# Kernel tuning notes

Measured on AMD Instinct MI355X. Metric: run time of the kernel, lower is better.

The kernel has to match this reference:

```python
import jax, jax.numpy as jnp
import numpy as np

B, N_IN, N_UP, SEQ, CIN, COUT = 8, 7056, 28224, 9, 64, 32
E = 3 * N_UP  # nnz of sparse upsample matrix


def setup_inputs() -> dict:
    key = jax.random.key(0)
    ks = jax.random.split(key, 7)
    x = jax.random.normal(ks[0], (B, N_IN, CIN), dtype=jnp.float32)
    val = jax.random.uniform(ks[1], (E,), dtype=jnp.float32)
    # xavier-uniform-ish init for Linear(SEQ*CIN -> COUT)
    lim = float(np.sqrt(6.0 / (SEQ * CIN + COUT)))
    W = jax.random.uniform(ks[2], (SEQ * CIN, COUT), minval=-lim, maxval=lim, dtype=jnp.float32)
    b = jnp.zeros((COUT,), dtype=jnp.float32)
    row = jax.random.randint(ks[3], (E,), 0, N_UP)
    col = jax.random.randint(ks[4], (E,), 0, N_IN)
    indices = jax.random.randint(ks[5], (N_UP, SEQ), 0, N_UP)
    return {"x": x, "val": val, "W": W, "b": b, "row": row, "col": col, "indices": indices}


def reference(x, val, W, b, row, col, indices):
    # Pool: out[b, row, :] += x[b, col, :] * val   (sparse upsample, dim_size = N_UP)
    gathered = x[:, col, :] * val[None, :, None]              # [B, E, CIN]
    pooled = jnp.zeros((x.shape[0], N_UP, x.shape[2]), dtype=x.dtype)
    pooled = pooled.at[:, row, :].add(gathered)               # [B, N_UP, CIN]
    # SpiralConv: spiral neighborhood gather then Linear + ReLU
    spiral = pooled[:, indices.reshape(-1), :]                # [B, N_UP*SEQ, CIN]
    spiral = spiral.reshape(x.shape[0], N_UP, SEQ * x.shape[2])  # [B, N_UP, SEQ*CIN]
    out = jnp.einsum('bnf,fo->bno', spiral, W) + b            # [B, N_UP, COUT]
    return jax.nn.relu(out)
```

## Files before the change

### kernel.cpp

```cpp
#include <hip/hip_runtime.h>
#include <hip/hip_bf16.h>

namespace {
constexpr int kB    = 8;
constexpr int kNIn  = 7056;
constexpr int kNUp  = 28224;
constexpr int kSeq  = 9;
constexpr int kCin  = 64;
constexpr int kCout = 32;
constexpr int kE    = 3 * kNUp;
constexpr int kMRows = kB * kNUp;
constexpr int kTilesPerB = kNUp / 16;
constexpr int kWFragN = 18 * 2 * 64 * 8;
constexpr int kCap   = 24;

constexpr size_t kOffPool   = 0;
constexpr size_t kOffWfrag  = 28901376;
constexpr size_t kOffCur    = kOffWfrag + 36864;
constexpr size_t kOffBucket = kOffCur + 112896;
}

typedef __attribute__((ext_vector_type(8))) short short8;
typedef __attribute__((ext_vector_type(4))) float f32x4;

__device__ __forceinline__ unsigned short f32_to_bf16(float f) {
    unsigned int u = __float_as_uint(f);
    u += 0x7fffu + ((u >> 16) & 1u);
    return (unsigned short)(u >> 16);
}

__global__ __launch_bounds__(256) void zero_kernel(int* __restrict__ cursor) {
    int i = blockIdx.x * 256 + threadIdx.x;
    if (i < kNUp) cursor[i] = 0;
}

__global__ __launch_bounds__(256) void prep_kernel(const float* __restrict__ W,
                                                   unsigned short* __restrict__ wfrag,
                                                   const int* __restrict__ row,
                                                   const int* __restrict__ col,
                                                   const float* __restrict__ val,
                                                   int* __restrict__ cursor,
                                                   uint2* __restrict__ bucket) {
    int bid = blockIdx.x;
    if (bid < kWFragN / 256) {
        int i  = bid * 256 + threadIdx.x;
        int j  = i & 7;
        int l  = (i >> 3) & 63;
        int ct = (i >> 9) & 1;
        int ks = i >> 10;
        int k  = ks * 32 + (l >> 4) * 8 + j;
        int o  = ct * 16 + (l & 15);
        wfrag[i] = f32_to_bf16(W[k * kCout + o]);
    } else {
        int e = (bid - kWFragN / 256) * 256 + threadIdx.x;
        if (e >= kE) return;
        int r = row[e];
        int slot = atomicAdd(&cursor[r], 1);
        if ((unsigned)slot < (unsigned)kCap)
            bucket[(size_t)r * kCap + slot] = make_uint2((unsigned)col[e], __float_as_uint(val[e]));
    }
}

__global__ __launch_bounds__(256) void pool_gather(const float* __restrict__ x,
                                                   const int* __restrict__ cursor,
                                                   const uint2* __restrict__ bucket,
                                                   unsigned short* __restrict__ poolb) {
    int t  = threadIdx.x;
    int c4 = t & 15;
    int b  = blockIdx.x & 7;
    int rb = blockIdx.x >> 3;
    int r  = rb * 16 + (t >> 4);
    int n  = min(cursor[r], kCap);
    const uint2* bk = bucket + (size_t)r * kCap;
    const float* xb = x + (size_t)b * kNIn * kCin + (size_t)c4 * 4;

    f32x4 acc = {0.f, 0.f, 0.f, 0.f};

#pragma unroll
    for (int p = 0; p < 4; ++p) {
        if (2 * p < n) {
            uint4 q = *reinterpret_cast<const uint4*>(bk + 2 * p);
            unsigned c0 = min(q.x, (unsigned)(kNIn - 1));
            float    v0 = __uint_as_float(q.y);
            unsigned c1 = min(q.z, (unsigned)(kNIn - 1));
            float    v1 = (2 * p + 1 < n) ? __uint_as_float(q.w) : 0.f;
            f32x4 xv0 = *reinterpret_cast<const f32x4*>(xb + (size_t)c0 * kCin);
            f32x4 xv1 = *reinterpret_cast<const f32x4*>(xb + (size_t)c1 * kCin);
#pragma unroll
            for (int j = 0; j < 4; ++j)
                acc[j] = fmaf(xv1[j], v1, fmaf(xv0[j], v0, acc[j]));
        }
    }
    for (int k = 8; k < n; ++k) {
        uint2 ev = bk[k];
        float v = __uint_as_float(ev.y);
        f32x4 xv = *reinterpret_cast<const f32x4*>(xb + (size_t)ev.x * kCin);
#pragma unroll
        for (int j = 0; j < 4; ++j)
            acc[j] = fmaf(xv[j], v, acc[j]);
    }

    ushort4 o;
    o.x = f32_to_bf16(acc[0]);
    o.y = f32_to_bf16(acc[1]);
    o.z = f32_to_bf16(acc[2]);
    o.w = f32_to_bf16(acc[3]);
    *reinterpret_cast<ushort4*>(poolb + ((size_t)b * kNUp + r) * kCin + c4 * 4) = o;
}

__global__ __launch_bounds__(256) void gemm_mfma(const unsigned short* __restrict__ poolb,
                                                 const unsigned short* __restrict__ wfrag,
                                                 const float* __restrict__ bias,
                                                 const int* __restrict__ indices,
                                                 float* __restrict__ out) {
    __shared__ short8 Bs[18 * 2 * 64];
    int t = threadIdx.x;
    const short8* wf = (const short8*)wfrag;
#pragma unroll
    for (int i = 0; i < 9; ++i)
        Bs[i * 256 + t] = wf[i * 256 + t];

    int l = t & 63;
    int w = t >> 6;
    int bid = blockIdx.x;
    int wk = (bid & 7) * (gridDim.x >> 3) + (bid >> 3);
    int mtile = wk * 4 + w;
    int m  = l & 15;
    int kg = l >> 4;
    int b  = mtile / kTilesPerB;
    int nn = (mtile - b * kTilesPerB) * 16 + m;
    const unsigned short* pb = poolb + (size_t)b * kNUp * kCin;

    int idxs[kSeq];
#pragma unroll
    for (int s = 0; s < kSeq; ++s) idxs[s] = indices[nn * kSeq + s];

    short8 A0[kSeq], A1[kSeq];
#pragma unroll
    for (int s = 0; s < kSeq; ++s) {
        const short8* arow = (const short8*)(pb + (size_t)idxs[s] * kCin);
        A0[s] = arow[kg];
        A1[s] = arow[4 + kg];
    }
    float bs0 = bias[m];
    float bs1 = bias[16 + m];

    __syncthreads();

    f32x4 acc0 = {0.f, 0.f, 0.f, 0.f};
    f32x4 acc1 = {0.f, 0.f, 0.f, 0.f};
#pragma unroll
    for (int s = 0; s < kSeq; ++s) {
        short8 b00 = Bs[((s * 2 + 0) * 2 + 0) * 64 + l];
        short8 b01 = Bs[((s * 2 + 0) * 2 + 1) * 64 + l];
        short8 b10 = Bs[((s * 2 + 1) * 2 + 0) * 64 + l];
        short8 b11 = Bs[((s * 2 + 1) * 2 + 1) * 64 + l];
        acc0 = __builtin_amdgcn_mfma_f32_16x16x32_bf16(A0[s], b00, acc0, 0, 0, 0);
        acc1 = __builtin_amdgcn_mfma_f32_16x16x32_bf16(A0[s], b01, acc1, 0, 0, 0);
        acc0 = __builtin_amdgcn_mfma_f32_16x16x32_bf16(A1[s], b10, acc0, 0, 0, 0);
        acc1 = __builtin_amdgcn_mfma_f32_16x16x32_bf16(A1[s], b11, acc1, 0, 0, 0);
    }

    int orow0 = mtile * 16 + kg * 4;
#pragma unroll
    for (int r = 0; r < 4; ++r) {
        size_t orow = (size_t)(orow0 + r) * kCout;
        out[orow + m]      = fmaxf(acc0[r] + bs0, 0.f);
        out[orow + 16 + m] = fmaxf(acc1[r] + bs1, 0.f);
    }
}

extern "C" void kernel_launch(void* const* d_in, const int* in_sizes, int n_in,
                              void* d_out, int out_size, void* d_ws, size_t ws_size,
                              hipStream_t stream) {
    const float* x    = (const float*)d_in[0];
    const float* val  = (const float*)d_in[1];
    const float* W    = (const float*)d_in[2];
    const float* bias = (const float*)d_in[3];
    const int* row     = (const int*)d_in[4];
    const int* col     = (const int*)d_in[5];
    const int* indices = (const int*)d_in[6];
    float* out = (float*)d_out;

    char* wsb = (char*)d_ws;
    unsigned short* poolb = (unsigned short*)(wsb + kOffPool);
    unsigned short* wfrag = (unsigned short*)(wsb + kOffWfrag);
    int* cursor  = (int*)(wsb + kOffCur);
    uint2* bucket = (uint2*)(wsb + kOffBucket);

    zero_kernel<<<(kNUp + 255) / 256, 256, 0, stream>>>(cursor);

    constexpr int prep_blocks = kWFragN / 256 + (kE + 255) / 256;
    prep_kernel<<<prep_blocks, 256, 0, stream>>>(W, wfrag, row, col, val, cursor, bucket);

    pool_gather<<<kNUp / 16 * kB, 256, 0, stream>>>(x, cursor, bucket, poolb);

    gemm_mfma<<<(kMRows / 16) / 4, 256, 0, stream>>>(poolb, wfrag, bias, indices, out);
}
```

Before: 76.34 us.

## Process four M-tiles per wave with software-pipelined spiral gathers in GEMM

```diff
diff --git a/kernel.cpp b/kernel.cpp
--- a/kernel.cpp
+++ b/kernel.cpp
@@ -13,6 +13,7 @@
 constexpr int kTilesPerB = kNUp / 16;
 constexpr int kWFragN = 18 * 2 * 64 * 8;
 constexpr int kCap   = 24;
+constexpr int kGemmGrid = kMRows / 16 / 16;
 
 constexpr size_t kOffPool   = 0;
 constexpr size_t kOffWfrag  = 28901376;
@@ -122,51 +123,84 @@
 
     int l = t & 63;
     int w = t >> 6;
-    int bid = blockIdx.x;
-    int wk = (bid & 7) * (gridDim.x >> 3) + (bid >> 3);
-    int mtile = wk * 4 + w;
     int m  = l & 15;
     int kg = l >> 4;
-    int b  = mtile / kTilesPerB;
-    int nn = (mtile - b * kTilesPerB) * 16 + m;
-    const unsigned short* pb = poolb + (size_t)b * kNUp * kCin;
-
-    int idxs[kSeq];
-#pragma unroll
-    for (int s = 0; s < kSeq; ++s) idxs[s] = indices[nn * kSeq + s];
-
-    short8 A0[kSeq], A1[kSeq];
-#pragma unroll
-    for (int s = 0; s < kSeq; ++s) {
-        const short8* arow = (const short8*)(pb + (size_t)idxs[s] * kCin);
-        A0[s] = arow[kg];
-        A1[s] = arow[4 + kg];
+
+    int bid = blockIdx.x;
+    int xcd = bid & 7;
+    int loc = bid >> 3;
+    int wgid = (xcd < 2 ? xcd * 111 : 222 + (xcd - 2) * 110) + loc;
+
+    int mbase = wgid * 16 + w * 4;
+
+    const unsigned short* pbp[4];
+    int idxs[4][kSeq];
+#pragma unroll
+    for (int tt = 0; tt < 4; ++tt) {
+        int mt = mbase + tt;
+        int bb = mt / kTilesPerB;
+        int n  = (mt - bb * kTilesPerB) * 16 + m;
+        pbp[tt] = poolb + (size_t)bb * kNUp * kCin;
+#pragma unroll
+        for (int s = 0; s < kSeq; ++s) idxs[tt][s] = indices[n * kSeq + s];
     }
     float bs0 = bias[m];
     float bs1 = bias[16 + m];
 
+    short8 A0[4], A1[4], N0[4], N1[4];
+#pragma unroll
+    for (int tt = 0; tt < 4; ++tt) {
+        const short8* ar = (const short8*)(pbp[tt] + (size_t)idxs[tt][0] * kCin);
+        A0[tt] = ar[kg];
+        A1[tt] = ar[4 + kg];
+    }
+
+    f32x4 acc0[4], acc1[4];
+#pragma unroll
+    for (int tt = 0; tt < 4; ++tt) {
+        acc0[tt] = (f32x4){0.f, 0.f, 0.f, 0.f};
+        acc1[tt] = (f32x4){0.f, 0.f, 0.f, 0.f};
+    }
+
     __syncthreads();
 
-    f32x4 acc0 = {0.f, 0.f, 0.f, 0.f};
-    f32x4 acc1 = {0.f, 0.f, 0.f, 0.f};
 #pragma unroll
     for (int s = 0; s < kSeq; ++s) {
-        short8 b00 = Bs[((s * 2 + 0) * 2 + 0) * 64 + l];
-        short8 b01 = Bs[((s * 2 + 0) * 2 + 1) * 64 + l];
-        short8 b10 = Bs[((s * 2 + 1) * 2 + 0) * 64 + l];
-        short8 b11 = Bs[((s * 2 + 1) * 2 + 1) * 64 + l];
-        acc0 = __builtin_amdgcn_mfma_f32_16x16x32_bf16(A0[s], b00, acc0, 0, 0, 0);
-        acc1 = __builtin_amdgcn_mfma_f32_16x16x32_bf16(A0[s], b01, acc1, 0, 0, 0);
-        acc0 = __builtin_amdgcn_mfma_f32_16x16x32_bf16(A1[s], b10, acc0, 0, 0, 0);
-        acc1 = __builtin_amdgcn_mfma_f32_16x16x32_bf16(A1[s], b11, acc1, 0, 0, 0);
-    }
-
-    int orow0 = mtile * 16 + kg * 4;
-#pragma unroll
-    for (int r = 0; r < 4; ++r) {
-        size_t orow = (size_t)(orow0 + r) * kCout;
-        out[orow + m]      = fmaxf(acc0[r] + bs0, 0.f);
-        out[orow + 16 + m] = fmaxf(acc1[r] + bs1, 0.f);
+        if (s < kSeq - 1) {
+#pragma unroll
+            for (int tt = 0; tt < 4; ++tt) {
+                const short8* ar = (const short8*)(pbp[tt] + (size_t)idxs[tt][s + 1] * kCin);
+                N0[tt] = ar[kg];
+                N1[tt] = ar[4 + kg];
+            }
+        }
+        short8 b00 = Bs[(4 * s + 0) * 64 + l];
+        short8 b01 = Bs[(4 * s + 1) * 64 + l];
+        short8 b10 = Bs[(4 * s + 2) * 64 + l];
+        short8 b11 = Bs[(4 * s + 3) * 64 + l];
+#pragma unroll
+        for (int tt = 0; tt < 4; ++tt) {
+            acc0[tt] = __builtin_amdgcn_mfma_f32_16x16x32_bf16(A0[tt], b00, acc0[tt], 0, 0, 0);
+            acc1[tt] = __builtin_amdgcn_mfma_f32_16x16x32_bf16(A0[tt], b01, acc1[tt], 0, 0, 0);
+            acc0[tt] = __builtin_amdgcn_mfma_f32_16x16x32_bf16(A1[tt], b10, acc0[tt], 0, 0, 0);
+            acc1[tt] = __builtin_amdgcn_mfma_f32_16x16x32_bf16(A1[tt], b11, acc1[tt], 0, 0, 0);
+        }
+#pragma unroll
+        for (int tt = 0; tt < 4; ++tt) {
+            A0[tt] = N0[tt];
+            A1[tt] = N1[tt];
+        }
+    }
+
+#pragma unroll
+    for (int tt = 0; tt < 4; ++tt) {
+        int orow0 = (mbase + tt) * 16 + kg * 4;
+#pragma unroll
+        for (int r = 0; r < 4; ++r) {
+            size_t orow = (size_t)(orow0 + r) * kCout;
+            out[orow + m]      = fmaxf(acc0[tt][r] + bs0, 0.f);
+            out[orow + 16 + m] = fmaxf(acc1[tt][r] + bs1, 0.f);
+        }
     }
 }
 
@@ -195,5 +229,5 @@
 
     pool_gather<<<kNUp / 16 * kB, 256, 0, stream>>>(x, cursor, bucket, poolb);
 
-    gemm_mfma<<<(kMRows / 16) / 4, 256, 0, stream>>>(poolb, wfrag, bias, indices, out);
-}
+    gemm_mfma<<<kGemmGrid, 256, 0, stream>>>(poolb, wfrag, bias, indices, out);
+}
```

New measurement: 78.42 us. +2.7%, slower.
